# Optimization experiments

Hardware: AMD Instinct MI355X
Metric: run time of the kernel (lower is better)

Reference implementation:

```python
import math
import jax, jax.numpy as jnp
import numpy as np

INPUT_DIM = 1024
HEADS = 16
SEQ = 4096
BATCH = 1
SCALE = math.sqrt(INPUT_DIM / HEADS)  # 8.0


def setup_inputs() -> dict:
    key = jax.random.key(0)
    ks = jax.random.split(key, 5)
    D = INPUT_DIM
    return {
        "x": jax.random.normal(ks[0], (BATCH, SEQ, D), dtype=jnp.float32),
        "w_qkv": jax.random.normal(ks[1], (3 * D, D), dtype=jnp.float32) * (1.0 / math.sqrt(D)),
        "b_qkv": jax.random.normal(ks[2], (3 * D,), dtype=jnp.float32) * 0.01,
        "w_out": jax.random.normal(ks[3], (D, D), dtype=jnp.float32) * (1.0 / math.sqrt(D)),
        "b_out": jax.random.normal(ks[4], (D,), dtype=jnp.float32) * 0.01,
    }


def reference(x, w_qkv, b_qkv, w_out, b_out):
    b, n, D = x.shape
    h = HEADS
    d = D // h
    # qkv projection: [b, n, 3D]
    qkv = x @ w_qkv.T + b_qkv
    # 'b n (c h d) -> b c h n d' with c=3 outermost
    qkv = qkv.reshape(b, n, 3, h, d).transpose(2, 0, 3, 1, 4)  # [3, b, h, n, d]
    q, k, v = qkv[0], qkv[1], qkv[2]
    q = q / SCALE
    attn = jnp.einsum('bhnd,bhmd->bhnm', q, k)  # [b, h, n, n]
    attn = jax.nn.softmax(attn, axis=-1)
    # dropout is identity in eval mode
    context = jnp.einsum('bhnm,bhmd->bhnd', attn, v)  # [b, h, n, d]
    context = context.transpose(0, 2, 1, 3).reshape(b, n, D)  # 'b h n d -> b n (h d)'
    return context @ w_out.T + b_out
```

## Files before the change

### kernel.cpp

```cpp
#include <hip/hip_runtime.h>

typedef unsigned short u16;
typedef unsigned int u32;
typedef __attribute__((ext_vector_type(8))) short short8;
typedef __attribute__((ext_vector_type(4))) float f32x4;

__device__ __forceinline__ u16 f2b(float f) {
  union { float f; unsigned u; } v; v.f = f;
  unsigned r = (v.u + 0x7FFFu + ((v.u >> 16) & 1u)) >> 16;
  return (u16)r;
}
__device__ __forceinline__ float b2f(u16 b) {
  union { unsigned u; float f; } v; v.u = ((unsigned)b) << 16;
  return v.f;
}
__device__ __forceinline__ u32 cvtpk(float a, float b) {
  u32 r;
  asm("v_cvt_pk_bf16_f32 %0, %1, %2" : "=v"(r) : "v"(a), "v"(b));
  return r;
}
__device__ __forceinline__ void p32swap(u32& a, u32& b) {
  asm("v_permlane32_swap_b32 %0, %1" : "+v"(a), "+v"(b));
}
__device__ __forceinline__ void p16swap(u32& a, u32& b) {
  asm("v_permlane16_swap_b32 %0, %1" : "+v"(a), "+v"(b));
}
__device__ __forceinline__ float ldf(const void* p, size_t i, int f32) {
  return f32 ? ((const float*)p)[i] : b2f(((const u16*)p)[i]);
}

__global__ __launch_bounds__(256) void detect_dtype(const u16* __restrict__ x,
                                                    int* __restrict__ flag) {
  __shared__ int cnt;
  if (threadIdx.x == 0) cnt = 0;
  __syncthreads();
  int local = 0;
  for (int p = threadIdx.x; p < 512; p += 256) {
    int e = (x[2 * p] >> 7) & 0xFF;
    if (e >= 0xC0) local++;
  }
  atomicAdd(&cnt, local);
  __syncthreads();
  if (threadIdx.x == 0) flag[0] = (cnt >= 16) ? 1 : 0;
}

__global__ __launch_bounds__(256) void convert_all(
    const void* __restrict__ px, const void* __restrict__ pwq,
    const void* __restrict__ pbq, const void* __restrict__ pwo,
    const void* __restrict__ pbo, u16* __restrict__ xb,
    u16* __restrict__ wqkvb, u16* __restrict__ bqkvb, u16* __restrict__ wob,
    u16* __restrict__ bob) {
  __shared__ int sf;
  if (threadIdx.x == 0) sf = 0;
  __syncthreads();
  {
    const u16* xr = (const u16*)px;
    int local = 0;
    for (int p = threadIdx.x; p < 512; p += 256) {
      int e = (xr[2 * p] >> 7) & 0xFF;
      if (e >= 0xC0) local++;
    }
    atomicAdd(&sf, local);
  }
  __syncthreads();
  const int isf32 = (sf >= 16);

  int i = blockIdx.x * 256 + threadIdx.x;
  const void* in; u16* out; size_t g;
  if (i < 524288)       { in = px;  out = xb;    g = (size_t)i; }
  else if (i < 917504)  { in = pwq; out = wqkvb; g = (size_t)(i - 524288); }
  else if (i < 917888)  { in = pbq; out = bqkvb; g = (size_t)(i - 917504); }
  else if (i < 1048960) { in = pwo; out = wob;   g = (size_t)(i - 917888); }
  else                  { in = pbo; out = bob;   g = (size_t)(i - 1048960); }
  size_t base = g * 8;
  if (isf32) {
    const float* p = (const float*)in + base;
    float4 v0 = *(const float4*)p, v1 = *(const float4*)(p + 4);
    union { short8 v; u16 e[8]; } t;
    t.e[0]=f2b(v0.x); t.e[1]=f2b(v0.y); t.e[2]=f2b(v0.z); t.e[3]=f2b(v0.w);
    t.e[4]=f2b(v1.x); t.e[5]=f2b(v1.y); t.e[6]=f2b(v1.z); t.e[7]=f2b(v1.w);
    *(short8*)(out + base) = t.v;
  } else {
    *(short8*)(out + base) = *(const short8*)((const u16*)in + base);
  }
}

__global__ __launch_bounds__(256) void transpose_v(const u16* __restrict__ qkv,
                                                   u16* __restrict__ Vt) {
  __shared__ u16 T[64 * 72];
  const int tid = threadIdx.x;
  const int h = blockIdx.y;
  const int s0 = blockIdx.x * 64;
  for (int r = 0; r < 2; ++r) {
    int cid = r * 256 + tid;
    int s = cid >> 3, c8 = cid & 7;
    union { short8 v; u16 u[8]; } uu;
    uu.v = *(const short8*)(qkv + (size_t)(s0 + s) * 3072 + 2048 + h * 64 + c8 * 8);
    for (int i = 0; i < 8; ++i) T[(c8 * 8 + i) * 72 + s] = uu.u[i];
  }
  __syncthreads();
  for (int r = 0; r < 2; ++r) {
    int cid = r * 256 + tid;
    int dd = cid >> 3, c8 = cid & 7;
    union { short8 v; u16 u[8]; } uu;
    for (int i = 0; i < 8; ++i) uu.u[i] = T[dd * 72 + c8 * 8 + i];
    *(short8*)(Vt + (size_t)(h * 64 + dd) * 4096 + s0 + c8 * 8) = uu.v;
  }
}

__global__ __launch_bounds__(256) void gemm_bt(const void* __restrict__ A,
                                               const void* __restrict__ B,
                                               const void* __restrict__ bias,
                                               void* __restrict__ C,
                                               int M, int N, int K,
                                               int lda, int ldb, int ldc,
                                               int aMay, int bMay, int outF32,
                                               const int* __restrict__ flag) {
  __shared__ __align__(16) u16 sm[128 * 132];
  u16* As = sm;
  u16* Bs = sm + 128 * 64;
  const int f = flag[0];
  const int a32 = aMay && f, b32 = bMay && f;
  const int tid = threadIdx.x;
  const int w = tid >> 6, lane = tid & 63;
  const int lq = lane & 15, qr = lane >> 4;
  const int m0 = blockIdx.y * 128, n0 = blockIdx.x * 128;
  const int wm = (w >> 1) * 64, wn = (w & 1) * 64;

  f32x4 acc[4][4];
  for (int i = 0; i < 4; i++)
    for (int j = 0; j < 4; j++) acc[i][j] = (f32x4){0.f, 0.f, 0.f, 0.f};
  float bv[4];
  for (int ns = 0; ns < 4; ++ns) bv[ns] = ldf(bias, n0 + wn + ns * 16 + lq, b32);

  const int rs = tid >> 3, cs = tid & 7;
  const u16* gA = (const u16*)A + (size_t)(m0 + rs) * lda + cs * 8;
  const u16* gB = (const u16*)B + (size_t)(n0 + rs) * ldb + cs * 8;
  u16* lA = As + ((tid & ~63) << 3);
  u16* lB = Bs + ((tid & ~63) << 3);

  for (int k0 = 0; k0 < K; k0 += 64) {
    if (!(a32 | b32)) {
      for (int r = 0; r < 4; ++r) {
        __builtin_amdgcn_global_load_lds(gA + (size_t)(r * 32) * lda + k0,
                                         lA + r * 2048, 16, 0, 0);
        __builtin_amdgcn_global_load_lds(gB + (size_t)(r * 32) * ldb + k0,
                                         lB + r * 2048, 16, 0, 0);
      }
    } else {
      for (int r = 0; r < 4; ++r) {
        int cid = r * 256 + tid;
        int row = cid >> 3, c = cid & 7;
        if (a32) {
          const float* p = (const float*)A + (size_t)(m0 + row) * lda + k0 + c * 8;
          float4 v0 = *(const float4*)p, v1 = *(const float4*)(p + 4);
          union { short8 v; u16 e[8]; } t;
          t.e[0]=f2b(v0.x); t.e[1]=f2b(v0.y); t.e[2]=f2b(v0.z); t.e[3]=f2b(v0.w);
          t.e[4]=f2b(v1.x); t.e[5]=f2b(v1.y); t.e[6]=f2b(v1.z); t.e[7]=f2b(v1.w);
          *(short8*)(As + row * 64 + c * 8) = t.v;
        } else {
          *(short8*)(As + row * 64 + c * 8) =
              *(const short8*)((const u16*)A + (size_t)(m0 + row) * lda + k0 + c * 8);
        }
        if (b32) {
          const float* p = (const float*)B + (size_t)(n0 + row) * ldb + k0 + c * 8;
          float4 v0 = *(const float4*)p, v1 = *(const float4*)(p + 4);
          union { short8 v; u16 e[8]; } t;
          t.e[0]=f2b(v0.x); t.e[1]=f2b(v0.y); t.e[2]=f2b(v0.z); t.e[3]=f2b(v0.w);
          t.e[4]=f2b(v1.x); t.e[5]=f2b(v1.y); t.e[6]=f2b(v1.z); t.e[7]=f2b(v1.w);
          *(short8*)(Bs + row * 64 + c * 8) = t.v;
        } else {
          *(short8*)(Bs + row * 64 + c * 8) =
              *(const short8*)((const u16*)B + (size_t)(n0 + row) * ldb + k0 + c * 8);
        }
      }
    }
    __syncthreads();
    for (int ks = 0; ks < 2; ++ks) {
      short8 af[4], bf[4];
      const int sw = ks * 4 + qr;
      for (int i = 0; i < 4; i++) {
        af[i] = *(const short8*)(As + (wm + i * 16 + lq) * 64 + sw * 8);
        bf[i] = *(const short8*)(Bs + (wn + i * 16 + lq) * 64 + sw * 8);
      }
      for (int mi = 0; mi < 4; mi++)
        for (int ni = 0; ni < 4; ni++)
          acc[mi][ni] = __builtin_amdgcn_mfma_f32_16x16x32_bf16(
              af[mi], bf[ni], acc[mi][ni], 0, 0, 0);
    }
    __syncthreads();
  }

  if (!outF32) {
    u16* SH = sm;
    for (int mi = 0; mi < 4; mi++)
      for (int ni = 0; ni < 4; ni++)
        for (int r = 0; r < 4; ++r)
          SH[(wm + mi * 16 + qr * 4 + r) * 132 + wn + ni * 16 + lq] =
              f2b(acc[mi][ni][r] + bv[ni]);
    __syncthreads();
    for (int it = 0; it < 8; ++it) {
      int idx = it * 256 + tid;
      int row = idx >> 4, c8 = idx & 15;
      *(short8*)((u16*)C + (size_t)(m0 + row) * ldc + n0 + c8 * 8) =
          *(const short8*)(SH + row * 132 + c8 * 8);
    }
  } else {
    float* SHf = (float*)sm;
    for (int half = 0; half < 2; ++half) {
      if (half) __syncthreads();
      if ((w >> 1) == half) {
        for (int mi = 0; mi < 4; mi++)
          for (int ni = 0; ni < 4; ni++)
            for (int r = 0; r < 4; ++r)
              SHf[(mi * 16 + qr * 4 + r) * 132 + wn + ni * 16 + lq] =
                  acc[mi][ni][r] + bv[ni];
      }
      __syncthreads();
      for (int it = 0; it < 8; ++it) {
        int idx = it * 256 + tid;
        int row = idx >> 5, c4 = idx & 31;
        *(float4*)((float*)C + (size_t)(m0 + half * 64 + row) * ldc + n0 + c4 * 4) =
            *(const float4*)(SHf + row * 132 + c4 * 4);
      }
    }
  }
}

__global__ __launch_bounds__(512, 2) void attn_split(const u16* __restrict__ qkv,
                                                     const u16* __restrict__ Vtg,
                                                     u16* __restrict__ ctx, int ldctx) {
  __shared__ __align__(16) u16 SMEM[2][16384];
  const int tid = threadIdx.x;
  const int w = tid >> 6, lane = tid & 63;
  const int half = w >> 2, wq = w & 3, wl = w & 3;
  const int lq = lane & 15, qr = lane >> 4;
  const int qb = blockIdx.x, h = blockIdx.y;
  const int qbase = qb * 128 + wq * 32;
  const float cs = 0.18033688011112042f;

  short8 qf[2][2];
#pragma unroll
  for (int mi = 0; mi < 2; ++mi)
#pragma unroll
    for (int ks = 0; ks < 2; ++ks)
      qf[mi][ks] = *(const short8*)(qkv + (size_t)(qbase + mi * 16 + lq) * 3072 +
                                    h * 64 + ks * 32 + qr * 8);

  f32x4 o[2][4];
#pragma unroll
  for (int mi = 0; mi < 2; ++mi)
#pragma unroll
    for (int ds = 0; ds < 4; ++ds) o[mi][ds] = (f32x4){0.f, 0.f, 0.f, 0.f};
  float lrow[2] = {0.f, 0.f};

  const int csw = ((lane & 7) ^ (lane >> 3)) << 3;
  const int r0v = wl * 8 + (lane >> 3);
  const u16* sK0 = qkv + (size_t)(half * 2048 + r0v) * 3072 + 1024 + h * 64 + csw;
  const u16* sK1 = sK0 + (size_t)32 * 3072;
  const u16* sV0 = Vtg + (size_t)(h * 64 + r0v) * 4096 + half * 2048 + csw;
  const u16* sV1 = sV0 + (size_t)32 * 4096;
  const int kb = half * 4096 + wl * 512;
  const int vb = 8192 + half * 4096 + wl * 512;

#define STAGE(buf)                                                          \
  do {                                                                      \
    u16* B_ = &SMEM[buf][0];                                                \
    __builtin_amdgcn_global_load_lds(sK0, B_ + kb, 16, 0, 0);               \
    __builtin_amdgcn_global_load_lds(sK1, B_ + kb + 2048, 16, 0, 0);        \
    __builtin_amdgcn_global_load_lds(sV0, B_ + vb, 16, 0, 0);               \
    __builtin_amdgcn_global_load_lds(sV1, B_ + vb + 2048, 16, 0, 0);        \
    sK0 += (size_t)64 * 3072; sK1 += (size_t)64 * 3072;                     \
    sV0 += 64; sV1 += 64;                                                   \
  } while (0)

  STAGE(0);
  __syncthreads();

  for (int it = 0; it < 32; ++it) {
    const int cur = it & 1;
    if (it + 1 < 32) STAGE(cur ^ 1);
    const u16* Kh = &SMEM[cur][half * 4096];
    const u16* Vh = &SMEM[cur][8192 + half * 4096];

    f32x4 s[2][4];
#pragma unroll
    for (int mi = 0; mi < 2; ++mi)
#pragma unroll
      for (int ns = 0; ns < 4; ++ns) s[mi][ns] = (f32x4){0.f, 0.f, 0.f, 0.f};
#pragma unroll
    for (int ks = 0; ks < 2; ++ks) {
      short8 kf[4];
#pragma unroll
      for (int ns = 0; ns < 4; ++ns) {
        int rk = ns * 16 + lq;
        kf[ns] = *(const short8*)(Kh + rk * 64 + (((ks * 4 + qr) ^ (lq & 7)) << 3));
      }
      __builtin_amdgcn_s_setprio(1);
#pragma unroll
      for (int mi = 0; mi < 2; ++mi)
#pragma unroll
        for (int ns = 0; ns < 4; ++ns)
          s[mi][ns] = __builtin_amdgcn_mfma_f32_16x16x32_bf16(
              kf[ns], qf[mi][ks], s[mi][ns], 0, 0, 0);
      __builtin_amdgcn_s_setprio(0);
    }

    short8 pf[2][2];
#pragma unroll
    for (int mi = 0; mi < 2; ++mi) {
      float lacc = 0.f;
      u32 X[4], Y[4];
#pragma unroll
      for (int ns = 0; ns < 4; ++ns) {
        float p0 = __builtin_amdgcn_exp2f(fmaf(s[mi][ns][0], cs, -12.0f));
        float p1 = __builtin_amdgcn_exp2f(fmaf(s[mi][ns][1], cs, -12.0f));
        float p2 = __builtin_amdgcn_exp2f(fmaf(s[mi][ns][2], cs, -12.0f));
        float p3 = __builtin_amdgcn_exp2f(fmaf(s[mi][ns][3], cs, -12.0f));
        lacc += (p0 + p1) + (p2 + p3);
        X[ns] = cvtpk(p0, p1);
        Y[ns] = cvtpk(p2, p3);
      }
      lrow[mi] += lacc;
#pragma unroll
      for (int ks = 0; ks < 2; ++ks) {
        u32 a0 = X[2 * ks], b0 = X[2 * ks + 1];
        u32 a1 = Y[2 * ks], b1 = Y[2 * ks + 1];
        p32swap(a0, b0); p16swap(a0, b0);
        p32swap(a1, b1); p16swap(a1, b1);
        union { u32 u[4]; short8 v; } t;
        t.u[0] = a0; t.u[1] = a1; t.u[2] = b0; t.u[3] = b1;
        pf[mi][ks] = t.v;
      }
    }

#pragma unroll
    for (int ks = 0; ks < 2; ++ks) {
      short8 vf[4];
#pragma unroll
      for (int ds = 0; ds < 4; ++ds) {
        int dv = ds * 16 + lq;
        vf[ds] = *(const short8*)(Vh + (size_t)dv * 64 +
                                  (((ks * 4 + qr) ^ (lq & 7)) << 3));
      }
      __builtin_amdgcn_s_setprio(1);
#pragma unroll
      for (int mi = 0; mi < 2; ++mi)
#pragma unroll
        for (int ds = 0; ds < 4; ++ds)
          o[mi][ds] = __builtin_amdgcn_mfma_f32_16x16x32_bf16(
              vf[ds], pf[mi][ks], o[mi][ds], 0, 0, 0);
      __builtin_amdgcn_s_setprio(0);
    }
    __syncthreads();
  }
#undef STAGE

  float* CB = (float*)&SMEM[0][0];
#pragma unroll
  for (int mi = 0; mi < 2; ++mi) {
    float* p = CB + (size_t)(wq * 64 + lane) * 17;
    if (half == 1) {
#pragma unroll
      for (int ds = 0; ds < 4; ++ds) {
        p[ds * 4 + 0] = o[mi][ds][0];
        p[ds * 4 + 1] = o[mi][ds][1];
        p[ds * 4 + 2] = o[mi][ds][2];
        p[ds * 4 + 3] = o[mi][ds][3];
      }
      p[16] = lrow[mi];
    }
    __syncthreads();
    if (half == 0) {
#pragma unroll
      for (int ds = 0; ds < 4; ++ds) {
        o[mi][ds][0] += p[ds * 4 + 0];
        o[mi][ds][1] += p[ds * 4 + 1];
        o[mi][ds][2] += p[ds * 4 + 2];
        o[mi][ds][3] += p[ds * 4 + 3];
      }
      lrow[mi] += p[16];
    }
    __syncthreads();
  }

  if (half == 0) {
#pragma unroll
    for (int mi = 0; mi < 2; ++mi) {
      float l = lrow[mi];
      l += __shfl_xor(l, 16, 64);
      l += __shfl_xor(l, 32, 64);
      float linv = 1.f / fmaxf(l, 1e-30f);
      int row = qbase + mi * 16 + lq;
      u16* dst = ctx + (size_t)row * ldctx + h * 64 + qr * 4;
#pragma unroll
      for (int ds = 0; ds < 4; ++ds) {
        u32 lo = cvtpk(o[mi][ds][0] * linv, o[mi][ds][1] * linv);
        u32 hi = cvtpk(o[mi][ds][2] * linv, o[mi][ds][3] * linv);
        *(uint2*)(dst + ds * 16) = make_uint2(lo, hi);
      }
    }
  }
}

__global__ __launch_bounds__(256) void attn_fused(const u16* __restrict__ qkv,
                                                  const u16* __restrict__ Vtg,
                                                  u16* __restrict__ ctx, int ldctx) {
  __shared__ u16 Ks[64 * 64];
  __shared__ u16 Vts[64 * 64];
  const int tid = threadIdx.x;
  const int w = tid >> 6, lane = tid & 63;
  const int lq = lane & 15, qr = lane >> 4;
  const int qb = blockIdx.x, h = blockIdx.y;
  const int qbase = qb * 128 + w * 32;
  const float cs = 0.18033688011112042f;

  short8 qf[2][2];
  for (int mi = 0; mi < 2; ++mi)
    for (int ks = 0; ks < 2; ++ks)
      qf[mi][ks] = *(const short8*)(qkv + (size_t)(qbase + mi * 16 + lq) * 3072 +
                                    h * 64 + ks * 32 + qr * 8);

  f32x4 o[2][4];
  for (int mi = 0; mi < 2; ++mi)
    for (int ds = 0; ds < 4; ++ds) o[mi][ds] = (f32x4){0.f, 0.f, 0.f, 0.f};
  float lrow[2] = {0.f, 0.f};

  const int c = tid & 7, r0 = tid >> 3;
  u16* dKA = Ks + r0 * 64 + ((c ^ (r0 & 7)) << 3);
  u16* dKB = dKA + 32 * 64;
  u16* dVA = Vts + r0 * 64 + ((c ^ (r0 & 7)) << 3);
  u16* dVB = dVA + 32 * 64;
  const u16* sKA = qkv + (size_t)r0 * 3072 + 1024 + h * 64 + c * 8;
  const u16* sKB = sKA + (size_t)32 * 3072;
  const u16* sVA = Vtg ? (Vtg + (size_t)(h * 64 + r0) * 4096 + c * 8) : nullptr;
  const u16* sVB = Vtg ? (sVA + (size_t)32 * 4096) : nullptr;
  const u16* sVfA = qkv + (size_t)r0 * 3072 + 2048 + h * 64 + c * 8;
  const u16* sVfB = sVfA + (size_t)32 * 3072;

  short8 rKA, rKB, rVA, rVB;
  union { short8 v; u16 e[8]; } ufA, ufB;
  rKA = *(const short8*)sKA; sKA += (size_t)64 * 3072;
  rKB = *(const short8*)sKB; sKB += (size_t)64 * 3072;
  if (Vtg) {
    rVA = *(const short8*)sVA; sVA += 64;
    rVB = *(const short8*)sVB; sVB += 64;
  } else {
    ufA.v = *(const short8*)sVfA; sVfA += (size_t)64 * 3072;
    ufB.v = *(const short8*)sVfB; sVfB += (size_t)64 * 3072;
  }

  for (int j0 = 0; j0 < 4096; j0 += 64) {
    __syncthreads();
    *(short8*)dKA = rKA;
    *(short8*)dKB = rKB;
    if (Vtg) {
      *(short8*)dVA = rVA;
      *(short8*)dVB = rVB;
    } else {
      {
        const int jc = r0 >> 3;
        for (int i = 0; i < 8; ++i)
          Vts[(c * 8 + i) * 64 + ((jc ^ i) << 3) + (r0 & 7)] = ufA.e[i];
      }
      {
        const int jc = (r0 + 32) >> 3;
        for (int i = 0; i < 8; ++i)
          Vts[(c * 8 + i) * 64 + ((jc ^ i) << 3) + (r0 & 7)] = ufB.e[i];
      }
    }
    __syncthreads();

    if (j0 + 64 < 4096) {
      rKA = *(const short8*)sKA; sKA += (size_t)64 * 3072;
      rKB = *(const short8*)sKB; sKB += (size_t)64 * 3072;
      if (Vtg) {
        rVA = *(const short8*)sVA; sVA += 64;
        rVB = *(const short8*)sVB; sVB += 64;
      } else {
        ufA.v = *(const short8*)sVfA; sVfA += (size_t)64 * 3072;
        ufB.v = *(const short8*)sVfB; sVfB += (size_t)64 * 3072;
      }
    }

    f32x4 s[2][4];
    for (int mi = 0; mi < 2; ++mi)
      for (int ns = 0; ns < 4; ++ns) s[mi][ns] = (f32x4){0.f, 0.f, 0.f, 0.f};
    for (int ks = 0; ks < 2; ++ks) {
      short8 kf[4];
      for (int ns = 0; ns < 4; ++ns) {
        int rk = ns * 16 + lq;
        kf[ns] = *(const short8*)(Ks + rk * 64 + (((ks * 4 + qr) ^ (lq & 7)) << 3));
      }
      __builtin_amdgcn_s_setprio(1);
      for (int mi = 0; mi < 2; ++mi)
        for (int ns = 0; ns < 4; ++ns)
          s[mi][ns] = __builtin_amdgcn_mfma_f32_16x16x32_bf16(
              kf[ns], qf[mi][ks], s[mi][ns], 0, 0, 0);
      __builtin_amdgcn_s_setprio(0);
    }

    short8 pf[2][2];
#pragma unroll
    for (int mi = 0; mi < 2; ++mi) {
      float lacc = 0.f;
      u32 X[4], Y[4];
#pragma unroll
      for (int ns = 0; ns < 4; ++ns) {
        float p0 = __builtin_amdgcn_exp2f(fmaf(s[mi][ns][0], cs, -12.0f));
        float p1 = __builtin_amdgcn_exp2f(fmaf(s[mi][ns][1], cs, -12.0f));
        float p2 = __builtin_amdgcn_exp2f(fmaf(s[mi][ns][2], cs, -12.0f));
        float p3 = __builtin_amdgcn_exp2f(fmaf(s[mi][ns][3], cs, -12.0f));
        lacc += (p0 + p1) + (p2 + p3);
        X[ns] = cvtpk(p0, p1);
        Y[ns] = cvtpk(p2, p3);
      }
      lrow[mi] += lacc;
#pragma unroll
      for (int ks = 0; ks < 2; ++ks) {
        u32 a0 = X[2 * ks], b0 = X[2 * ks + 1];
        u32 a1 = Y[2 * ks], b1 = Y[2 * ks + 1];
        p32swap(a0, b0); p16swap(a0, b0);
        p32swap(a1, b1); p16swap(a1, b1);
        union { u32 u[4]; short8 v; } t;
        t.u[0] = a0; t.u[1] = a1; t.u[2] = b0; t.u[3] = b1;
        pf[mi][ks] = t.v;
      }
    }

    for (int ks = 0; ks < 2; ++ks) {
      short8 vf[4];
      for (int ds = 0; ds < 4; ++ds) {
        int dv = ds * 16 + lq;
        vf[ds] = *(const short8*)(Vts + (size_t)dv * 64 +
                                  (((ks * 4 + qr) ^ (lq & 7)) << 3));
      }
      __builtin_amdgcn_s_setprio(1);
      for (int mi = 0; mi < 2; ++mi)
        for (int ds = 0; ds < 4; ++ds)
          o[mi][ds] = __builtin_amdgcn_mfma_f32_16x16x32_bf16(
              vf[ds], pf[mi][ks], o[mi][ds], 0, 0, 0);
      __builtin_amdgcn_s_setprio(0);
    }
  }

  for (int mi = 0; mi < 2; ++mi) {
    float l = lrow[mi];
    l += __shfl_xor(l, 16, 64);
    l += __shfl_xor(l, 32, 64);
    float linv = 1.f / fmaxf(l, 1e-30f);
    int row = qbase + mi * 16 + lq;
    u16* dst = ctx + (size_t)row * ldctx + h * 64 + qr * 4;
    for (int ds = 0; ds < 4; ++ds) {
      u32 lo = cvtpk(o[mi][ds][0] * linv, o[mi][ds][1] * linv);
      u32 hi = cvtpk(o[mi][ds][2] * linv, o[mi][ds][3] * linv);
      *(uint2*)(dst + ds * 16) = make_uint2(lo, hi);
    }
  }
}

extern "C" void kernel_launch(void* const* d_in, const int* in_sizes, int n_in,
                              void* d_out, int out_size, void* d_ws, size_t ws_size,
                              hipStream_t stream) {
  float* out = (float*)d_out;

  const void *px = nullptr, *pwq = nullptr, *pbq = nullptr, *pwo = nullptr, *pbo = nullptr;
  if (n_in == 5) {
    for (int i = 0; i < 5; ++i) {
      switch (in_sizes[i]) {
        case 4194304: px = d_in[i]; break;
        case 3145728: pwq = d_in[i]; break;
        case 3072:    pbq = d_in[i]; break;
        case 1048576: pwo = d_in[i]; break;
        case 1024:    pbo = d_in[i]; break;
        default: break;
      }
    }
  }
  if (!px || !pwq || !pbq || !pwo || !pbo) {
    px = d_in[0]; pwq = d_in[1]; pbq = d_in[2]; pwo = d_in[3]; pbo = d_in[4];
  }

  int* flag = (int*)d_ws;
  u16* qkv = (u16*)((char*)d_ws + 64);
  u16* ctx = qkv;

  const size_t nQKV = (size_t)4096 * 3072;
  const size_t nVt = (size_t)16 * 64 * 4096;
  const size_t nx = 4194304, nwq = 3145728, nwo = 1048576;
  u16* Vtg = qkv + nQKV;
  const size_t need_vt = 64 + (nQKV + nVt) * 2;
  const size_t need_full = need_vt + (nx + nwq + 4096 + nwo + 1024) * 2;

  if (ws_size >= need_full) {
    u16* xb    = Vtg + nVt;
    u16* wqkvb = xb + nx;
    u16* bqkvb = wqkvb + nwq;
    u16* wob   = bqkvb + 4096;
    u16* bob   = wob + nwo;
    convert_all<<<4098, 256, 0, stream>>>(px, pwq, pbq, pwo, pbo,
                                          xb, wqkvb, bqkvb, wob, bob);

    gemm_bt<<<dim3(24, 32), 256, 0, stream>>>(xb, wqkvb, bqkvb, qkv,
                                              4096, 3072, 1024, 1024, 1024, 3072,
                                              0, 0, 0, flag);
    transpose_v<<<dim3(64, 16), 256, 0, stream>>>(qkv, Vtg);
    attn_split<<<dim3(32, 16), 512, 0, stream>>>(qkv, Vtg, ctx, 3072);
    gemm_bt<<<dim3(8, 32), 256, 0, stream>>>(ctx, wob, bob, out,
                                             4096, 1024, 1024, 3072, 1024, 1024,
                                             0, 0, 1, flag);
  } else if (ws_size >= need_vt) {
    detect_dtype<<<1, 256, 0, stream>>>((const u16*)px, flag);
    gemm_bt<<<dim3(24, 32), 256, 0, stream>>>(px, pwq, pbq, qkv,
                                              4096, 3072, 1024, 1024, 1024, 3072,
                                              1, 1, 0, flag);
    transpose_v<<<dim3(64, 16), 256, 0, stream>>>(qkv, Vtg);
    attn_split<<<dim3(32, 16), 512, 0, stream>>>(qkv, Vtg, ctx, 3072);
    gemm_bt<<<dim3(8, 32), 256, 0, stream>>>(ctx, pwo, pbo, out,
                                             4096, 1024, 1024, 3072, 1024, 1024,
                                             0, 1, 1, flag);
  } else {
    detect_dtype<<<1, 256, 0, stream>>>((const u16*)px, flag);
    gemm_bt<<<dim3(24, 32), 256, 0, stream>>>(px, pwq, pbq, qkv,
                                              4096, 3072, 1024, 1024, 1024, 3072,
                                              1, 1, 0, flag);
    attn_fused<<<dim3(32, 16), 256, 0, stream>>>(qkv, (const u16*)nullptr, ctx, 3072);
    gemm_bt<<<dim3(8, 32), 256, 0, stream>>>(ctx, pwo, pbo, out,
                                             4096, 1024, 1024, 3072, 1024, 1024,
                                             0, 1, 1, flag);
  }
}
```

Baseline: 257.6 us.

## Add intra-block split-K output projection GEMM and write fp32 output directly

Adds a 512-thread output-projection GEMM in which two halves of the block each handle half of K and then reduce their partial sums through shared memory, which doubles the waves per tile for the small 256-block launch. The fp32 epilogue of the generic GEMM now stores directly from registers instead of staging through LDS. The attn_fused path drops its unused Vtg branch. The in-block reduction adds LDS traffic and barriers, and the direct stores are less coalesced than the staged ones.

```diff
diff --git a/kernel.cpp b/kernel.cpp
--- a/kernel.cpp
+++ b/kernel.cpp
@@ -206,22 +206,97 @@
           *(const short8*)(SH + row * 132 + c8 * 8);
     }
   } else {
-    float* SHf = (float*)sm;
-    for (int half = 0; half < 2; ++half) {
-      if (half) __syncthreads();
-      if ((w >> 1) == half) {
-        for (int mi = 0; mi < 4; mi++)
-          for (int ni = 0; ni < 4; ni++)
-            for (int r = 0; r < 4; ++r)
-              SHf[(mi * 16 + qr * 4 + r) * 132 + wn + ni * 16 + lq] =
-                  acc[mi][ni][r] + bv[ni];
-      }
-      __syncthreads();
-      for (int it = 0; it < 8; ++it) {
-        int idx = it * 256 + tid;
-        int row = idx >> 5, c4 = idx & 31;
-        *(float4*)((float*)C + (size_t)(m0 + half * 64 + row) * ldc + n0 + c4 * 4) =
-            *(const float4*)(SHf + row * 132 + c4 * 4);
+    float* Cf = (float*)C;
+    for (int mi = 0; mi < 4; mi++) {
+      int row = m0 + wm + mi * 16 + qr * 4;
+      for (int r = 0; r < 4; ++r) {
+        float* rp = Cf + (size_t)(row + r) * ldc + n0 + wn;
+        for (int ni = 0; ni < 4; ni++)
+          rp[ni * 16 + lq] = acc[mi][ni][r] + bv[ni];
+      }
+    }
+  }
+}
+
+__global__ __launch_bounds__(512, 2) void gemm_bt_ks(const u16* __restrict__ A,
+                                                     const u16* __restrict__ B,
+                                                     const u16* __restrict__ bias,
+                                                     float* __restrict__ C,
+                                                     int K, int lda, int ldb, int ldc) {
+  __shared__ __align__(16) u16 sm[2][16384];
+  const int tid = threadIdx.x;
+  const int w = tid >> 6, lane = tid & 63;
+  const int half = w >> 2, wq = w & 3;
+  const int ht = tid & 255;
+  const int lq = lane & 15, qr = lane >> 4;
+  const int m0 = blockIdx.y * 128, n0 = blockIdx.x * 128;
+  const int wm = (wq >> 1) * 64, wn = (wq & 1) * 64;
+  const int kh = K >> 1;
+
+  u16* As = &sm[half][0];
+  u16* Bs = &sm[half][8192];
+
+  f32x4 acc[4][4];
+  for (int i = 0; i < 4; i++)
+    for (int j = 0; j < 4; j++) acc[i][j] = (f32x4){0.f, 0.f, 0.f, 0.f};
+  float bv[4];
+  for (int ns = 0; ns < 4; ++ns) bv[ns] = b2f(bias[n0 + wn + ns * 16 + lq]);
+
+  const int rs = ht >> 3, cs = ht & 7;
+  const u16* gA = A + (size_t)(m0 + rs) * lda + half * kh + cs * 8;
+  const u16* gB = B + (size_t)(n0 + rs) * ldb + half * kh + cs * 8;
+  u16* lA = As + ((ht & ~63) << 3);
+  u16* lB = Bs + ((ht & ~63) << 3);
+
+  for (int k0 = 0; k0 < kh; k0 += 64) {
+    for (int r = 0; r < 4; ++r) {
+      __builtin_amdgcn_global_load_lds(gA + (size_t)(r * 32) * lda + k0,
+                                       lA + r * 2048, 16, 0, 0);
+      __builtin_amdgcn_global_load_lds(gB + (size_t)(r * 32) * ldb + k0,
+                                       lB + r * 2048, 16, 0, 0);
+    }
+    __syncthreads();
+    for (int ks = 0; ks < 2; ++ks) {
+      short8 af[4], bf[4];
+      const int sw = ks * 4 + qr;
+      for (int i = 0; i < 4; i++) {
+        af[i] = *(const short8*)(As + (wm + i * 16 + lq) * 64 + sw * 8);
+        bf[i] = *(const short8*)(Bs + (wn + i * 16 + lq) * 64 + sw * 8);
+      }
+      for (int mi = 0; mi < 4; mi++)
+        for (int ni = 0; ni < 4; ni++)
+          acc[mi][ni] = __builtin_amdgcn_mfma_f32_16x16x32_bf16(
+              af[mi], bf[ni], acc[mi][ni], 0, 0, 0);
+    }
+    __syncthreads();
+  }
+
+  float* CB = (float*)&sm[0][0];
+  float* p = CB + (size_t)ht * 33;
+  for (int t = 0; t < 2; ++t) {
+    if (half == 1) {
+      for (int u = 0; u < 2; ++u)
+        for (int ni = 0; ni < 4; ++ni)
+          for (int r = 0; r < 4; ++r)
+            p[u * 16 + ni * 4 + r] = acc[2 * t + u][ni][r];
+    }
+    __syncthreads();
+    if (half == 0) {
+      for (int u = 0; u < 2; ++u)
+        for (int ni = 0; ni < 4; ++ni)
+          for (int r = 0; r < 4; ++r)
+            acc[2 * t + u][ni][r] += p[u * 16 + ni * 4 + r];
+    }
+    __syncthreads();
+  }
+
+  if (half == 0) {
+    for (int mi = 0; mi < 4; mi++) {
+      int row = m0 + wm + mi * 16 + qr * 4;
+      for (int r = 0; r < 4; ++r) {
+        float* rp = C + (size_t)(row + r) * ldc + n0 + wn;
+        for (int ni = 0; ni < 4; ni++)
+          rp[ni * 16 + lq] = acc[mi][ni][r] + bv[ni];
       }
     }
   }
@@ -429,58 +504,39 @@
   const int c = tid & 7, r0 = tid >> 3;
   u16* dKA = Ks + r0 * 64 + ((c ^ (r0 & 7)) << 3);
   u16* dKB = dKA + 32 * 64;
-  u16* dVA = Vts + r0 * 64 + ((c ^ (r0 & 7)) << 3);
-  u16* dVB = dVA + 32 * 64;
   const u16* sKA = qkv + (size_t)r0 * 3072 + 1024 + h * 64 + c * 8;
   const u16* sKB = sKA + (size_t)32 * 3072;
-  const u16* sVA = Vtg ? (Vtg + (size_t)(h * 64 + r0) * 4096 + c * 8) : nullptr;
-  const u16* sVB = Vtg ? (sVA + (size_t)32 * 4096) : nullptr;
   const u16* sVfA = qkv + (size_t)r0 * 3072 + 2048 + h * 64 + c * 8;
   const u16* sVfB = sVfA + (size_t)32 * 3072;
 
-  short8 rKA, rKB, rVA, rVB;
+  short8 rKA, rKB;
   union { short8 v; u16 e[8]; } ufA, ufB;
   rKA = *(const short8*)sKA; sKA += (size_t)64 * 3072;
   rKB = *(const short8*)sKB; sKB += (size_t)64 * 3072;
-  if (Vtg) {
-    rVA = *(const short8*)sVA; sVA += 64;
-    rVB = *(const short8*)sVB; sVB += 64;
-  } else {
-    ufA.v = *(const short8*)sVfA; sVfA += (size_t)64 * 3072;
-    ufB.v = *(const short8*)sVfB; sVfB += (size_t)64 * 3072;
-  }
+  ufA.v = *(const short8*)sVfA; sVfA += (size_t)64 * 3072;
+  ufB.v = *(const short8*)sVfB; sVfB += (size_t)64 * 3072;
 
   for (int j0 = 0; j0 < 4096; j0 += 64) {
     __syncthreads();
     *(short8*)dKA = rKA;
     *(short8*)dKB = rKB;
-    if (Vtg) {
-      *(short8*)dVA = rVA;
-      *(short8*)dVB = rVB;
-    } else {
-      {
-        const int jc = r0 >> 3;
-        for (int i = 0; i < 8; ++i)
-          Vts[(c * 8 + i) * 64 + ((jc ^ i) << 3) + (r0 & 7)] = ufA.e[i];
-      }
-      {
-        const int jc = (r0 + 32) >> 3;
-        for (int i = 0; i < 8; ++i)
-          Vts[(c * 8 + i) * 64 + ((jc ^ i) << 3) + (r0 & 7)] = ufB.e[i];
-      }
+    {
+      const int jc = r0 >> 3;
+      for (int i = 0; i < 8; ++i)
+        Vts[(c * 8 + i) * 64 + ((jc ^ i) << 3) + (r0 & 7)] = ufA.e[i];
+    }
+    {
+      const int jc = (r0 + 32) >> 3;
+      for (int i = 0; i < 8; ++i)
+        Vts[(c * 8 + i) * 64 + ((jc ^ i) << 3) + (r0 & 7)] = ufB.e[i];
     }
     __syncthreads();
 
     if (j0 + 64 < 4096) {
       rKA = *(const short8*)sKA; sKA += (size_t)64 * 3072;
       rKB = *(const short8*)sKB; sKB += (size_t)64 * 3072;
-      if (Vtg) {
-        rVA = *(const short8*)sVA; sVA += 64;
-        rVB = *(const short8*)sVB; sVB += 64;
-      } else {
-        ufA.v = *(const short8*)sVfA; sVfA += (size_t)64 * 3072;
-        ufB.v = *(const short8*)sVfB; sVfB += (size_t)64 * 3072;
-      }
+      ufA.v = *(const short8*)sVfA; sVfA += (size_t)64 * 3072;
+      ufB.v = *(const short8*)sVfB; sVfB += (size_t)64 * 3072;
     }
 
     f32x4 s[2][4];
@@ -606,9 +662,8 @@
                                               0, 0, 0, flag);
     transpose_v<<<dim3(64, 16), 256, 0, stream>>>(qkv, Vtg);
     attn_split<<<dim3(32, 16), 512, 0, stream>>>(qkv, Vtg, ctx, 3072);
-    gemm_bt<<<dim3(8, 32), 256, 0, stream>>>(ctx, wob, bob, out,
-                                             4096, 1024, 1024, 3072, 1024, 1024,
-                                             0, 0, 1, flag);
+    gemm_bt_ks<<<dim3(8, 32), 512, 0, stream>>>(ctx, wob, bob, out,
+                                                1024, 3072, 1024, 1024);
   } else if (ws_size >= need_vt) {
     detect_dtype<<<1, 256, 0, stream>>>((const u16*)px, flag);
     gemm_bt<<<dim3(24, 32), 256, 0, stream>>>(px, pwq, pbq, qkv,
```

Result: no change. 260.1 us (+1.0%).
